# Optimization experiments

Measured on AMD Instinct MI355X. Metric: run time of the kernel, lower is better.

## Reference

```python
import jax, jax.numpy as jnp
import numpy as np

DEPTH, DIM, M_DIM, K = 3, 16, 16, 8  # depth, emb_dim, EGNN m_dim default, num_nearest_neighbors
LN_EPS = 1e-5


def _gather(x, idx):
    # x: [B,L,...], idx: [B,L,K] -> [B,L,K,...] (per-batch neighbor gather)
    return jax.vmap(lambda xb, ib: xb[ib])(x, idx)


def _lin(k, fi, fo):
    k1, k2 = jax.random.split(k)
    lim = 1.0 / np.sqrt(fi)
    w = jax.random.uniform(k1, (fi, fo), minval=-lim, maxval=lim, dtype=jnp.float32)
    b = jax.random.uniform(k2, (fo,), minval=-lim, maxval=lim, dtype=jnp.float32)
    return w, b


def _stacked(k, fi, fo):
    ws, bs = zip(*[_lin(kk, fi, fo) for kk in jax.random.split(k, DEPTH)])
    return jnp.stack(ws), jnp.stack(bs)


def setup_inputs() -> dict:
    key = jax.random.key(0)
    ks = jax.random.split(key, 16)
    B, L, num_tokens = 16, 1024, 2
    edge_in = 2 * DIM + 1  # feats_i, feats_j, rel_dist
    inp = {}
    inp['coords'] = jax.random.normal(ks[0], (B, L, 3), dtype=jnp.float32) * 3.0
    inp['residues'] = jax.random.randint(ks[1], (B, L), 0, num_tokens)
    inp['lengths'] = jax.random.randint(ks[2], (B,), L // 2, L + 1)
    inp['token_emb'] = jax.random.normal(ks[3], (num_tokens, DIM), dtype=jnp.float32)
    inp['pos_emb'] = jax.random.normal(ks[4], (L, DIM), dtype=jnp.float32)
    inp['edge_w1'], inp['edge_b1'] = _stacked(ks[5], edge_in, edge_in * 2)
    inp['edge_w2'], inp['edge_b2'] = _stacked(ks[6], edge_in * 2, M_DIM)
    inp['coors_w1'], inp['coors_b1'] = _stacked(ks[7], M_DIM, M_DIM * 4)
    inp['coors_w2'], inp['coors_b2'] = _stacked(ks[8], M_DIM * 4, 1)
    inp['ln_g'] = jnp.ones((DEPTH, DIM), jnp.float32)
    inp['ln_b'] = jnp.zeros((DEPTH, DIM), jnp.float32)
    inp['node_w1'], inp['node_b1'] = _stacked(ks[9], DIM + M_DIM, DIM * 2)
    inp['node_w2'], inp['node_b2'] = _stacked(ks[10], DIM * 2, DIM)
    inp['final_w'], inp['final_b'] = _lin(ks[11], DIM, 3)
    return inp


def reference(coords, residues, lengths, token_emb, pos_emb,
              edge_w1, edge_b1, edge_w2, edge_b2,
              coors_w1, coors_b1, coors_w2, coors_b2,
              ln_g, ln_b, node_w1, node_b1, node_w2, node_b2,
              final_w, final_b):
    B, L, _ = coords.shape
    silu = jax.nn.silu
    mask = jnp.arange(L)[None, :] < lengths[:, None]                 # [B,L]
    pair_mask = mask[:, :, None] & mask[:, None, :]                  # [B,L,L]
    eye = jnp.eye(L, dtype=bool)
    # chain adjacency: i <-> i+1 where both endpoints are within length
    r = jnp.arange(L - 1)
    chain = jnp.zeros((L, L), bool).at[r, r + 1].set(True)
    chain = chain | chain.T
    adj = (chain[None] & pair_mask) & ~eye                           # [B,L,L]

    feats = token_emb[residues] + pos_emb[None, :L]                  # [B,L,D]
    coors = coords
    for d in range(DEPTH):
        # pairwise squared distances for kNN ranking (memory-bound)
        rel_dist_full = jnp.sum((coors[:, :, None] - coors[:, None, :]) ** 2, -1)  # [B,L,L]
        ranking = jnp.where(pair_mask, rel_dist_full, 1e5)
        ranking = jnp.where(eye, -1.0, ranking)   # self always selected first
        ranking = jnp.where(adj, 0.0, ranking)    # adjacency edges forced in
        _, idx = jax.lax.top_k(-ranking, K)                           # [B,L,K] smallest
        mask_j = _gather(mask, idx)
        emask = mask[:, :, None] & mask_j                             # [B,L,K] (valid_radius=inf)
        coors_j = _gather(coors, idx)                                 # [B,L,K,3]
        rel_coors = coors[:, :, None] - coors_j                       # [B,L,K,3]
        rel_dist = jnp.sum(rel_coors ** 2, -1, keepdims=True)         # [B,L,K,1]
        feats_j = _gather(feats, idx)                                 # [B,L,K,D]
        feats_i = jnp.broadcast_to(feats[:, :, None], feats_j.shape)
        edge_in = jnp.concatenate([feats_i, feats_j, rel_dist], -1)   # [B,L,K,2D+1]
        h = silu(edge_in @ edge_w1[d] + edge_b1[d])
        m_ij = silu(h @ edge_w2[d] + edge_b2[d])                      # [B,L,K,M]
        # equivariant coordinate update
        w = silu(m_ij @ coors_w1[d] + coors_b1[d]) @ coors_w2[d] + coors_b2[d]
        w = jnp.where(emask[..., None], w, 0.0)[..., 0]               # [B,L,K]
        coors = coors + jnp.einsum('blk,blkc->blc', w, rel_coors)
        # node update (norm_feats=True in EGNN_Network -> LayerNorm)
        m_i = jnp.sum(jnp.where(emask[..., None], m_ij, 0.0), 2)      # [B,L,M]
        mu = feats.mean(-1, keepdims=True)
        var = jnp.mean((feats - mu) ** 2, -1, keepdims=True)
        normed = (feats - mu) / jnp.sqrt(var + LN_EPS) * ln_g[d] + ln_b[d]
        nin = jnp.concatenate([normed, m_i], -1)                      # [B,L,D+M]
        feats = feats + (silu(nin @ node_w1[d] + node_b1[d]) @ node_w2[d] + node_b2[d])
    delta = feats @ final_w + final_b                                 # [B,L,3]
    return delta
```

## Files before the change

### kernel.cpp

```cpp
#include <hip/hip_runtime.h>
#include <math.h>

typedef unsigned long long u64;
typedef unsigned int u32;

#define NB 16
#define SL 1024
#define DIM 16
#define MDIM 16
#define KNN 8
#define CH 64
#define NHID 32
#define LN_EPS 1e-5f
#define PST 144

__device__ __forceinline__ float silu_f(float x) {
    const float e = __expf(-x);
    return x * __builtin_amdgcn_rcpf(1.0f + e);
}

__global__ __launch_bounds__(256) void init_kernel(
    const float* __restrict__ coords, const int* __restrict__ residues,
    const float* __restrict__ token_emb, const float* __restrict__ pos_emb,
    const float* __restrict__ w1tp, const float* __restrict__ g_eb1,
    float* __restrict__ coordsA, float* __restrict__ featsA,
    float* __restrict__ Pout)
{
    const int t = blockIdx.x * 256 + threadIdx.x;
    const int node = t >> 2;
    const int part = t & 3;
    const int l = node & (SL - 1);
    const int r = residues[node];
    float f[16];
    {
        const float4* te = (const float4*)(token_emb + (size_t)r * DIM);
        const float4* pe = (const float4*)(pos_emb + (size_t)l * DIM);
#pragma unroll
        for (int q = 0; q < 4; ++q) {
            float4 a = te[q], b4 = pe[q];
            f[4*q+0] = a.x + b4.x; f[4*q+1] = a.y + b4.y;
            f[4*q+2] = a.z + b4.z; f[4*q+3] = a.w + b4.w;
        }
    }
    if (part == 0) {
        float4* fo = (float4*)(featsA + (size_t)node * DIM);
#pragma unroll
        for (int q = 0; q < 4; ++q)
            fo[q] = make_float4(f[4*q], f[4*q+1], f[4*q+2], f[4*q+3]);
        coordsA[node * 3 + 0] = coords[node * 3 + 0];
        coordsA[node * 3 + 1] = coords[node * 3 + 1];
        coordsA[node * 3 + 2] = coords[node * 3 + 2];
    }
    const int ubase = (part & 1) * 33;
    const int wbase = (part < 2) ? 0 : 66;
    float res[36];
    res[33] = 0.f; res[34] = 0.f; res[35] = 0.f;
#pragma unroll
    for (int oo = 0; oo < 33; ++oo) {
        const int u = ubase + oo;
        const float* wr = w1tp + (wbase + u) * 16;
        float a0 = (part < 2) ? g_eb1[u] : 0.0f;
        float a1 = 0.f, a2 = 0.f, a3 = 0.f;
#pragma unroll
        for (int c = 0; c < 16; c += 4) {
            a0 = fmaf(f[c + 0], wr[c + 0], a0);
            a1 = fmaf(f[c + 1], wr[c + 1], a1);
            a2 = fmaf(f[c + 2], wr[c + 2], a2);
            a3 = fmaf(f[c + 3], wr[c + 3], a3);
        }
        res[oo] = (a0 + a1) + (a2 + a3);
    }
    float4* op = (float4*)(Pout + (size_t)node * PST + part * 36);
#pragma unroll
    for (int q = 0; q < 9; ++q)
        op[q] = make_float4(res[4*q], res[4*q+1], res[4*q+2], res[4*q+3]);
}

__global__ __launch_bounds__(256) void pack_kernel(
    const float* __restrict__ ew1, const float* __restrict__ ew2,
    const float* __restrict__ cw1,
    const float* __restrict__ nw1, const float* __restrict__ nw2,
    float* __restrict__ w1tp, float* __restrict__ w1rp, float* __restrict__ w2p,
    float* __restrict__ cw1t, float* __restrict__ nw1t, float* __restrict__ nw2t)
{
    const int stride = gridDim.x * 256;
    const int t0 = blockIdx.x * 256 + threadIdx.x;
    for (int idx = t0; idx < 3 * 132 * 16; idx += stride) {
        int d = idx / (132 * 16); int r = idx - d * 132 * 16; int o = r >> 4; int c = r & 15;
        int u = (o < 66) ? o : (o - 66);
        int cc = (o < 66) ? c : (16 + c);
        w1tp[idx] = ew1[(d * 33 + cc) * 66 + u];
    }
    for (int idx = t0; idx < 3 * 72; idx += stride) {
        int d = idx / 72; int o = idx - d * 72; int hh = o / 36; int uu = o - hh * 36;
        w1rp[idx] = (uu < 33) ? ew1[(d * 33 + 32) * 66 + hh * 33 + uu] : 0.0f;
    }
    for (int idx = t0; idx < 3 * 72 * 16; idx += stride) {
        int d = idx / (72 * 16); int r = idx - d * 72 * 16; int u = r >> 4; int v = r & 15;
        int hh = u / 36; int uu = u - hh * 36;
        w2p[idx] = (uu < 33) ? ew2[(d * 66 + hh * 33 + uu) * 16 + v] : 0.0f;
    }
    for (int idx = t0; idx < 3 * CH * 16; idx += stride) {
        int d = idx / (CH * 16); int r = idx - d * CH * 16; int t = r >> 4; int v = r & 15;
        cw1t[(d * CH + t) * 16 + v] = cw1[(d * 16 + v) * CH + t];
    }
    for (int idx = t0; idx < 3 * NHID * 32; idx += stride) {
        int d = idx / (NHID * 32); int r = idx - d * NHID * 32; int u = r >> 5; int c = r & 31;
        nw1t[(d * NHID + u) * 32 + c] = nw1[(d * 32 + c) * NHID + u];
    }
    for (int idx = t0; idx < 3 * 16 * 32; idx += stride) {
        int d = idx / (16 * 32); int r = idx - d * 16 * 32; int c = r >> 5; int u = r & 31;
        nw2t[(d * 16 + c) * 32 + u] = nw2[(d * 32 + u) * 16 + c];
    }
}

__device__ __forceinline__ void merge8(u32* a, const u32* bb) {
    u32 c[8];
#pragma unroll
    for (int t = 0; t < 8; ++t) c[t] = min(a[t], bb[7 - t]);
#define MCAS(x, y) { u32 mn = min(c[x], c[y]); u32 mx = max(c[x], c[y]); c[x] = mn; c[y] = mx; }
    MCAS(0, 4) MCAS(1, 5) MCAS(2, 6) MCAS(3, 7)
    MCAS(0, 2) MCAS(1, 3) MCAS(4, 6) MCAS(5, 7)
    MCAS(0, 1) MCAS(2, 3) MCAS(4, 5) MCAS(6, 7)
#undef MCAS
#pragma unroll
    for (int t = 0; t < 8; ++t) a[t] = c[t];
}

__global__ __launch_bounds__(1024) void knn_kernel(
    const float* __restrict__ coords, const int* __restrict__ lengths,
    int* __restrict__ idxbuf)
{
    __shared__ __align__(16) float4 s_cand[SL];
    __shared__ u32 lists[16][64][9];
    const int tid = threadIdx.x;
    const int b = blockIdx.x >> 4;
    const int i0 = (blockIdx.x & 15) << 6;
    const int len = lengths[b];
    const float* cb = coords + (size_t)b * SL * 3;
    for (int idx = tid; idx < SL; idx += 1024) {
        const float* cp = cb + idx * 3;
        s_cand[idx] = make_float4(cp[0], cp[1], cp[2], 0.0f);
    }
    __syncthreads();

    const int wv = tid >> 6;
    const int lane = tid & 63;
    const int i = i0 + lane;
    const bool mi = i < len;
    const float4 qi = s_cand[i];
    const float xi = qi.x, yi = qi.y, zi = qi.z;

    u32 lst[8];
#pragma unroll
    for (int t = 0; t < 8; ++t) lst[t] = 0xFFFFFFFFu;

    const int jbase = wv << 6;
#pragma unroll 4
    for (int jj = 0; jj < 64; ++jj) {
        const int j = jbase + jj;
        const float4 cj = s_cand[j];
        const float dx = xi - cj.x, dy = yi - cj.y, dz = zi - cj.z;
        const float dist = dx * dx + dy * dy + dz * dz;
        const int dij = j - i;
        const bool pm = mi && (j < len);
        const bool adjx = (dij == 1) | (dij == -1);
        float v = pm ? (adjx ? 0.0f : dist) : 1e5f;
        v = (dij == 0) ? -1.0f : v;
        u32 bits = __float_as_uint(v);
        bits ^= (u32)((int)bits >> 31) | 0x80000000u;
        const u32 key = (bits & 0xFFFFFC00u) | (u32)j;
#pragma unroll
        for (int p = 7; p >= 1; --p)
            lst[p] = min(max(key, lst[p - 1]), lst[p]);
        lst[0] = min(key, lst[0]);
    }

#pragma unroll
    for (int t = 0; t < 8; ++t) lists[wv][lane][t] = lst[t];
    __syncthreads();

    if (tid < 512) {
        const int p = tid >> 6, q = tid & 63;
        u32 a[8], bb[8];
#pragma unroll
        for (int t = 0; t < 8; ++t) { a[t] = lists[2 * p][q][t]; bb[t] = lists[2 * p + 1][q][t]; }
        merge8(a, bb);
#pragma unroll
        for (int t = 0; t < 8; ++t) lists[2 * p][q][t] = a[t];
    }
    __syncthreads();
    if (tid < 256) {
        const int p = tid >> 6, q = tid & 63;
        u32 a[8], bb[8];
#pragma unroll
        for (int t = 0; t < 8; ++t) { a[t] = lists[4 * p][q][t]; bb[t] = lists[4 * p + 2][q][t]; }
        merge8(a, bb);
#pragma unroll
        for (int t = 0; t < 8; ++t) lists[4 * p][q][t] = a[t];
    }
    __syncthreads();
    if (tid < 128) {
        const int p = tid >> 6, q = tid & 63;
        u32 a[8], bb[8];
#pragma unroll
        for (int t = 0; t < 8; ++t) { a[t] = lists[8 * p][q][t]; bb[t] = lists[8 * p + 4][q][t]; }
        merge8(a, bb);
#pragma unroll
        for (int t = 0; t < 8; ++t) lists[8 * p][q][t] = a[t];
    }
    __syncthreads();
    if (tid < 64) {
        const int q = tid;
        u32 a[8], bb[8];
#pragma unroll
        for (int t = 0; t < 8; ++t) { a[t] = lists[0][q][t]; bb[t] = lists[8][q][t]; }
        merge8(a, bb);
        const size_t node = (size_t)b * SL + i0 + q;
        int4 r0 = make_int4((int)(a[0] & 1023u), (int)(a[1] & 1023u), (int)(a[2] & 1023u), (int)(a[3] & 1023u));
        int4 r1 = make_int4((int)(a[4] & 1023u), (int)(a[5] & 1023u), (int)(a[6] & 1023u), (int)(a[7] & 1023u));
        ((int4*)idxbuf)[node * 2 + 0] = r0;
        ((int4*)idxbuf)[node * 2 + 1] = r1;
    }
}

__global__ __launch_bounds__(256, 4) void layer_kernel(
    const int d,
    const float* __restrict__ coordsIn, float* __restrict__ coordsOut,
    const float* __restrict__ featsIn, float* __restrict__ featsOut,
    const float* __restrict__ Pbuf,
    const int* __restrict__ idxbuf, const int* __restrict__ lengths,
    const float* __restrict__ w1rp, const float* __restrict__ w2p,
    const float* __restrict__ g_eb2,
    const float* __restrict__ cw1t, const float* __restrict__ g_cb1,
    const float* __restrict__ g_cw2, const float* __restrict__ g_cb2,
    const float* __restrict__ g_lng, const float* __restrict__ g_lnb,
    const float* __restrict__ nw1t, const float* __restrict__ g_nb1,
    const float* __restrict__ nw2t, const float* __restrict__ g_nb2,
    const float* __restrict__ w1tp_all, const float* __restrict__ g_eb1,
    float* __restrict__ PbufOut)
{
    __shared__ float s_w2e[72 * 16];
    __shared__ float s_w1r[72];
    __shared__ float s_cw1[CH * 16];
    __shared__ float s_cw2v[CH];
    __shared__ float s_nw1[NHID * 36];
    __shared__ float s_nw2[16 * 36];
    __shared__ float s_eb2[16], s_cb1[CH];
    __shared__ float s_lng[16], s_lnb[16], s_nb1[32], s_nb2[16];
    __shared__ float s_cb2v;

    const int tid = threadIdx.x;
    for (int t = tid; t < 72 * 16; t += 256) s_w2e[t] = w2p[d * 72 * 16 + t];
    for (int t = tid; t < CH * 16; t += 256) s_cw1[t] = cw1t[d * CH * 16 + t];
    for (int t = tid; t < NHID * 32; t += 256) s_nw1[(t >> 5) * 36 + (t & 31)] = nw1t[d * NHID * 32 + t];
    for (int t = tid; t < 16 * 32; t += 256) s_nw2[(t >> 5) * 36 + (t & 31)] = nw2t[d * 16 * 32 + t];
    if (tid < 72) s_w1r[tid] = w1rp[d * 72 + tid];
    if (tid < CH) { s_cw2v[tid] = g_cw2[d * CH + tid]; s_cb1[tid] = g_cb1[d * CH + tid]; }
    if (tid < 16) {
        s_eb2[tid] = g_eb2[d * 16 + tid];
        s_lng[tid] = g_lng[d * 16 + tid];
        s_lnb[tid] = g_lnb[d * 16 + tid];
        s_nb2[tid] = g_nb2[d * 16 + tid];
    }
    if (tid < 32) s_nb1[tid] = g_nb1[d * 32 + tid];
    if (tid == 0) s_cb2v = g_cb2[d];

    const int lane = tid & 63;
    const int h = (lane >> 3) & 1;
    const int k = lane & 7;
    const int n = blockIdx.x * 16 + (tid >> 4);
    const int b = n >> 10;
    const int i = n & (SL - 1);
    const int len = lengths[b];
    const int j = idxbuf[n * 8 + k];
    const bool em = (i < len) && (j < len);

    float fi[16];
    {
        const float4* pp = (const float4*)(featsIn + (size_t)n * DIM);
        float4 a = pp[0], c2 = pp[1], c3 = pp[2], c4 = pp[3];
        fi[0]=a.x; fi[1]=a.y; fi[2]=a.z; fi[3]=a.w;
        fi[4]=c2.x; fi[5]=c2.y; fi[6]=c2.z; fi[7]=c2.w;
        fi[8]=c3.x; fi[9]=c3.y; fi[10]=c3.z; fi[11]=c3.w;
        fi[12]=c4.x; fi[13]=c4.y; fi[14]=c4.z; fi[15]=c4.w;
    }
    float ci[3], rel[3];
    {
        const float* cp = coordsIn + (size_t)n * 3;
        const float* cq = coordsIn + ((size_t)b * SL + j) * 3;
        ci[0] = cp[0]; ci[1] = cp[1]; ci[2] = cp[2];
        rel[0] = ci[0] - cq[0]; rel[1] = ci[1] - cq[1]; rel[2] = ci[2] - cq[2];
    }
    const float rd = fmaf(rel[0], rel[0], fmaf(rel[1], rel[1], rel[2] * rel[2]));

    const int ub = h * 36;
    const float* PiP = Pbuf + (size_t)n * PST + ub;
    const float* PjP = Pbuf + ((size_t)b * SL + j) * PST + 72 + ub;
    float4 pi_[9], pj_[9];
#pragma unroll
    for (int c4 = 0; c4 < 9; ++c4) {
        pi_[c4] = *(const float4*)(PiP + 4 * c4);
        pj_[c4] = *(const float4*)(PjP + 4 * c4);
    }

    __syncthreads();

    float macc[16];
#pragma unroll
    for (int v = 0; v < 16; ++v) macc[v] = h ? 0.0f : s_eb2[v];
#pragma unroll
    for (int c4 = 0; c4 < 9; ++c4) {
        const float4 pa = pi_[c4];
        const float4 pb = pj_[c4];
        const int u0 = ub + c4 * 4;
        const float hu0 = silu_f(fmaf(rd, s_w1r[u0 + 0], pa.x + pb.x));
        const float hu1 = silu_f(fmaf(rd, s_w1r[u0 + 1], pa.y + pb.y));
        const float hu2 = silu_f(fmaf(rd, s_w1r[u0 + 2], pa.z + pb.z));
        const float hu3 = silu_f(fmaf(rd, s_w1r[u0 + 3], pa.w + pb.w));
        const float* w2r = &s_w2e[u0 * 16];
#pragma unroll
        for (int v = 0; v < 16; ++v) {
            float m0 = fmaf(hu0, w2r[v], macc[v]);
            float m1 = fmaf(hu1, w2r[16 + v], m0);
            float m2 = fmaf(hu2, w2r[32 + v], m1);
            macc[v] = fmaf(hu3, w2r[48 + v], m2);
        }
    }

    float mm[16];
#pragma unroll
    for (int v = 0; v < 16; ++v)
        mm[v] = silu_f(macc[v] + __shfl_xor(macc[v], 8, 64));

    const int tb = h * 32;
    float wa = 0.f;
#pragma unroll 4
    for (int tt = 0; tt < 32; ++tt) {
        const float* cr = &s_cw1[(tb + tt) * 16];
        float a0 = s_cb1[tb + tt], a1 = 0.f;
#pragma unroll
        for (int v = 0; v < 16; v += 2) {
            a0 = fmaf(mm[v], cr[v], a0);
            a1 = fmaf(mm[v + 1], cr[v + 1], a1);
        }
        wa = fmaf(silu_f(a0 + a1), s_cw2v[tb + tt], wa);
    }
    const float wao = __shfl_xor(wa, 8, 64);
    const float we = em ? (wa + wao + s_cb2v) : 0.f;

    float wr0 = we * rel[0], wr1 = we * rel[1], wr2 = we * rel[2];
#pragma unroll
    for (int s = 1; s < 8; s <<= 1) {
        wr0 += __shfl_xor(wr0, s, 64);
        wr1 += __shfl_xor(wr1, s, 64);
        wr2 += __shfl_xor(wr2, s, 64);
    }
    if ((lane & 15) == 0) {
        coordsOut[(size_t)n * 3 + 0] = ci[0] + wr0;
        coordsOut[(size_t)n * 3 + 1] = ci[1] + wr1;
        coordsOut[(size_t)n * 3 + 2] = ci[2] + wr2;
    }

    float mi_[16];
#pragma unroll
    for (int v = 0; v < 16; ++v) mi_[v] = em ? mm[v] : 0.f;
#pragma unroll
    for (int s = 1; s < 8; s <<= 1) {
#pragma unroll
        for (int v = 0; v < 16; ++v) mi_[v] += __shfl_xor(mi_[v], s, 64);
    }

    float mu = 0.f;
#pragma unroll
    for (int c = 0; c < 16; ++c) mu += fi[c];
    mu *= 0.0625f;
    float var = 0.f;
#pragma unroll
    for (int c = 0; c < 16; ++c) { const float dd = fi[c] - mu; var = fmaf(dd, dd, var); }
    var *= 0.0625f;
    const float rs = rsqrtf(var + LN_EPS);
    float nn[16];
#pragma unroll
    for (int c = 0; c < 16; ++c) nn[c] = fmaf((fi[c] - mu) * rs, s_lng[c], s_lnb[c]);

    const int sub = lane & 15;
    float nh[2];
#pragma unroll
    for (int q = 0; q < 2; ++q) {
        const int u = sub * 2 + q;
        const float* nr = &s_nw1[u * 36];
        float a0 = s_nb1[u], a1 = 0.f;
#pragma unroll
        for (int c = 0; c < 16; c += 2) {
            a0 = fmaf(nn[c], nr[c], a0);
            a1 = fmaf(nn[c + 1], nr[c + 1], a1);
        }
#pragma unroll
        for (int v = 0; v < 16; v += 2) {
            a0 = fmaf(mi_[v], nr[16 + v], a0);
            a1 = fmaf(mi_[v + 1], nr[16 + v + 1], a1);
        }
        nh[q] = silu_f(a0 + a1);
    }

    const int nbase = lane & ~15;
    const float* w2c = &s_nw2[sub * 36];
    float o0 = s_nb2[sub];
#pragma unroll
    for (int u = 0; u < 32; ++u) {
        const float v = __shfl(nh[u & 1], nbase + (u >> 1), 64);
        o0 = fmaf(v, w2c[u], o0);
    }
    const float fo = fi[sub] + o0;
    featsOut[(size_t)n * DIM + sub] = fo;

    if (d < 2) {
        float fr[16];
#pragma unroll
        for (int c = 0; c < 16; ++c) fr[c] = __shfl(fo, nbase + c, 64);
        const float* wbase = w1tp_all + (d + 1) * 132 * 16;
        const float* bbase = g_eb1 + (d + 1) * 66;
        float* Pout = PbufOut + (size_t)n * PST;
#pragma unroll
        for (int q = 0; q < 9; ++q) {
            const int col = sub + (q << 4);
            const int ch = (col >= 108) ? 3 : (col >= 72) ? 2 : (col >= 36) ? 1 : 0;
            const int uu = col - ch * 36;
            const bool valid = uu < 33;
            const int u = ((ch & 1) ? 33 : 0) + uu;
            const int uc = valid ? u : 0;
            const int widx = valid ? ((ch < 2) ? u : 66 + u) : 0;
            float a0 = (valid && ch < 2) ? bbase[uc] : 0.0f;
            float a1 = 0.f, a2 = 0.f, a3 = 0.f;
            const float* wr = wbase + widx * 16;
#pragma unroll
            for (int cc = 0; cc < 16; cc += 4) {
                a0 = fmaf(fr[cc + 0], wr[cc + 0], a0);
                a1 = fmaf(fr[cc + 1], wr[cc + 1], a1);
                a2 = fmaf(fr[cc + 2], wr[cc + 2], a2);
                a3 = fmaf(fr[cc + 3], wr[cc + 3], a3);
            }
            Pout[col] = valid ? ((a0 + a1) + (a2 + a3)) : 0.0f;
        }
    }
}

__global__ __launch_bounds__(256) void final_kernel(
    const float* __restrict__ feats, const float* __restrict__ fw,
    const float* __restrict__ fb, float* __restrict__ out)
{
    const int nid = blockIdx.x * 256 + threadIdx.x;
    if (nid >= NB * SL) return;
    float f[DIM];
#pragma unroll
    for (int c = 0; c < DIM; ++c) f[c] = feats[nid * DIM + c];
#pragma unroll
    for (int o = 0; o < 3; ++o) {
        float acc = fb[o];
#pragma unroll
        for (int c = 0; c < DIM; ++c) acc = fmaf(f[c], fw[c * 3 + o], acc);
        out[nid * 3 + o] = acc;
    }
}

extern "C" void kernel_launch(void* const* d_in, const int* in_sizes, int n_in,
                              void* d_out, int out_size, void* d_ws, size_t ws_size,
                              hipStream_t stream) {
    const float* coords    = (const float*)d_in[0];
    const int*   residues  = (const int*)d_in[1];
    const int*   lengths   = (const int*)d_in[2];
    const float* token_emb = (const float*)d_in[3];
    const float* pos_emb   = (const float*)d_in[4];
    const float* ew1 = (const float*)d_in[5];
    const float* eb1 = (const float*)d_in[6];
    const float* ew2 = (const float*)d_in[7];
    const float* eb2 = (const float*)d_in[8];
    const float* cw1 = (const float*)d_in[9];
    const float* cb1 = (const float*)d_in[10];
    const float* cw2 = (const float*)d_in[11];
    const float* cb2 = (const float*)d_in[12];
    const float* lng = (const float*)d_in[13];
    const float* lnb = (const float*)d_in[14];
    const float* nw1 = (const float*)d_in[15];
    const float* nb1 = (const float*)d_in[16];
    const float* nw2 = (const float*)d_in[17];
    const float* nb2 = (const float*)d_in[18];
    const float* fw  = (const float*)d_in[19];
    const float* fb  = (const float*)d_in[20];

    float* ws = (float*)d_ws;
    float* coordsA = ws;
    float* coordsB = coordsA + NB * SL * 3;
    float* featsA  = coordsB + NB * SL * 3;
    float* featsB  = featsA + NB * SL * DIM;
    int*   idxbuf  = (int*)(featsB + NB * SL * DIM);
    float* w1tp = (float*)(idxbuf + NB * SL * KNN);
    float* w1rp = w1tp + 3 * 132 * 16;
    float* w2p  = w1rp + 3 * 72;
    float* cw1t = w2p + 3 * 72 * 16;
    float* nw1t = cw1t + 3 * CH * 16;
    float* nw2t = nw1t + 3 * NHID * 32;
    float* PbufA = nw2t + 3 * 16 * 32;
    float* PbufB = PbufA + (size_t)NB * SL * PST;

    pack_kernel<<<32, 256, 0, stream>>>(ew1, ew2, cw1, nw1, nw2, w1tp, w1rp, w2p, cw1t, nw1t, nw2t);
    init_kernel<<<NB * SL * 4 / 256, 256, 0, stream>>>(coords, residues, token_emb, pos_emb,
                                                        w1tp, eb1, coordsA, featsA, PbufA);

    float* cIn = coordsA; float* cOut = coordsB;
    float* fIn = featsA;  float* fOut = featsB;
    float* pIn = PbufA;   float* pOut = PbufB;
    for (int d = 0; d < 3; ++d) {
        knn_kernel<<<NB * SL / 64, 1024, 0, stream>>>(cIn, lengths, idxbuf);
        layer_kernel<<<NB * SL * KNN / 128, 256, 0, stream>>>(d, cIn, cOut, fIn, fOut, pIn, idxbuf, lengths,
            w1rp, w2p, eb2, cw1t, cb1, cw2, cb2, lng, lnb, nw1t, nb1, nw2t, nb2,
            w1tp, eb1, pOut);
        float* t;
        t = cIn; cIn = cOut; cOut = t;
        t = fIn; fIn = fOut; fOut = t;
        t = pIn; pIn = pOut; pOut = t;
    }

    final_kernel<<<NB * SL / 256, 256, 0, stream>>>(fIn, fw, fb, (float*)d_out);
}
```

Before: 281.2 us.

## Process two nodes per thread group in layer kernel to reuse shared weights

Each 16-lane group now handles two nodes (A and B, 16 apart), so every weight read from shared memory is reused for two independent FMA chains, and the grid is halved. The P-buffer float4 loads move into the compute loop and the w1r row is read as one aligned float4. This cuts LDS traffic per edge and adds independent work to hide latency. The cost is roughly double register use under launch_bounds(256,4), which may cause spills or lower occupancy, and fewer blocks.

```diff
diff --git a/kernel.cpp b/kernel.cpp
--- a/kernel.cpp
+++ b/kernel.cpp
@@ -241,7 +241,7 @@
     float* __restrict__ PbufOut)
 {
     __shared__ float s_w2e[72 * 16];
-    __shared__ float s_w1r[72];
+    __shared__ __align__(16) float s_w1r[72];
     __shared__ float s_cw1[CH * 16];
     __shared__ float s_cw2v[CH];
     __shared__ float s_nw1[NHID * 36];
@@ -269,159 +269,230 @@
     const int lane = tid & 63;
     const int h = (lane >> 3) & 1;
     const int k = lane & 7;
-    const int n = blockIdx.x * 16 + (tid >> 4);
-    const int b = n >> 10;
-    const int i = n & (SL - 1);
+    const int sub = lane & 15;
+    const int nA = blockIdx.x * 32 + (tid >> 4);
+    const int nB = nA + 16;
+    const int b = nA >> 10;
     const int len = lengths[b];
-    const int j = idxbuf[n * 8 + k];
-    const bool em = (i < len) && (j < len);
-
-    float fi[16];
+    const int jA = idxbuf[nA * 8 + k];
+    const int jB = idxbuf[nB * 8 + k];
+    const bool emA = ((nA & 1023) < len) && (jA < len);
+    const bool emB = ((nB & 1023) < len) && (jB < len);
+
+    float ciA[3], relA[3], ciB[3], relB[3];
     {
-        const float4* pp = (const float4*)(featsIn + (size_t)n * DIM);
-        float4 a = pp[0], c2 = pp[1], c3 = pp[2], c4 = pp[3];
-        fi[0]=a.x; fi[1]=a.y; fi[2]=a.z; fi[3]=a.w;
-        fi[4]=c2.x; fi[5]=c2.y; fi[6]=c2.z; fi[7]=c2.w;
-        fi[8]=c3.x; fi[9]=c3.y; fi[10]=c3.z; fi[11]=c3.w;
-        fi[12]=c4.x; fi[13]=c4.y; fi[14]=c4.z; fi[15]=c4.w;
-    }
-    float ci[3], rel[3];
-    {
-        const float* cp = coordsIn + (size_t)n * 3;
-        const float* cq = coordsIn + ((size_t)b * SL + j) * 3;
-        ci[0] = cp[0]; ci[1] = cp[1]; ci[2] = cp[2];
-        rel[0] = ci[0] - cq[0]; rel[1] = ci[1] - cq[1]; rel[2] = ci[2] - cq[2];
-    }
-    const float rd = fmaf(rel[0], rel[0], fmaf(rel[1], rel[1], rel[2] * rel[2]));
+        const float* cpA = coordsIn + (size_t)nA * 3;
+        const float* cqA = coordsIn + ((size_t)b * SL + jA) * 3;
+        ciA[0] = cpA[0]; ciA[1] = cpA[1]; ciA[2] = cpA[2];
+        relA[0] = ciA[0] - cqA[0]; relA[1] = ciA[1] - cqA[1]; relA[2] = ciA[2] - cqA[2];
+        const float* cpB = coordsIn + (size_t)nB * 3;
+        const float* cqB = coordsIn + ((size_t)b * SL + jB) * 3;
+        ciB[0] = cpB[0]; ciB[1] = cpB[1]; ciB[2] = cpB[2];
+        relB[0] = ciB[0] - cqB[0]; relB[1] = ciB[1] - cqB[1]; relB[2] = ciB[2] - cqB[2];
+    }
+    const float rdA = fmaf(relA[0], relA[0], fmaf(relA[1], relA[1], relA[2] * relA[2]));
+    const float rdB = fmaf(relB[0], relB[0], fmaf(relB[1], relB[1], relB[2] * relB[2]));
 
     const int ub = h * 36;
-    const float* PiP = Pbuf + (size_t)n * PST + ub;
-    const float* PjP = Pbuf + ((size_t)b * SL + j) * PST + 72 + ub;
-    float4 pi_[9], pj_[9];
+    const float* PiA = Pbuf + (size_t)nA * PST + ub;
+    const float* PjA = Pbuf + ((size_t)b * SL + jA) * PST + 72 + ub;
+    const float* PiB = Pbuf + (size_t)nB * PST + ub;
+    const float* PjB = Pbuf + ((size_t)b * SL + jB) * PST + 72 + ub;
+
+    __syncthreads();
+
+    float maccA[16], maccB[16];
+#pragma unroll
+    for (int v = 0; v < 16; ++v) {
+        const float e0 = h ? 0.0f : s_eb2[v];
+        maccA[v] = e0; maccB[v] = e0;
+    }
 #pragma unroll
     for (int c4 = 0; c4 < 9; ++c4) {
-        pi_[c4] = *(const float4*)(PiP + 4 * c4);
-        pj_[c4] = *(const float4*)(PjP + 4 * c4);
-    }
-
-    __syncthreads();
-
-    float macc[16];
-#pragma unroll
-    for (int v = 0; v < 16; ++v) macc[v] = h ? 0.0f : s_eb2[v];
-#pragma unroll
-    for (int c4 = 0; c4 < 9; ++c4) {
-        const float4 pa = pi_[c4];
-        const float4 pb = pj_[c4];
+        const float4 paA = *(const float4*)(PiA + 4 * c4);
+        const float4 pbA = *(const float4*)(PjA + 4 * c4);
+        const float4 paB = *(const float4*)(PiB + 4 * c4);
+        const float4 pbB = *(const float4*)(PjB + 4 * c4);
         const int u0 = ub + c4 * 4;
-        const float hu0 = silu_f(fmaf(rd, s_w1r[u0 + 0], pa.x + pb.x));
-        const float hu1 = silu_f(fmaf(rd, s_w1r[u0 + 1], pa.y + pb.y));
-        const float hu2 = silu_f(fmaf(rd, s_w1r[u0 + 2], pa.z + pb.z));
-        const float hu3 = silu_f(fmaf(rd, s_w1r[u0 + 3], pa.w + pb.w));
+        const float4 w1r4 = *(const float4*)&s_w1r[u0];
+        const float huA0 = silu_f(fmaf(rdA, w1r4.x, paA.x + pbA.x));
+        const float huA1 = silu_f(fmaf(rdA, w1r4.y, paA.y + pbA.y));
+        const float huA2 = silu_f(fmaf(rdA, w1r4.z, paA.z + pbA.z));
+        const float huA3 = silu_f(fmaf(rdA, w1r4.w, paA.w + pbA.w));
+        const float huB0 = silu_f(fmaf(rdB, w1r4.x, paB.x + pbB.x));
+        const float huB1 = silu_f(fmaf(rdB, w1r4.y, paB.y + pbB.y));
+        const float huB2 = silu_f(fmaf(rdB, w1r4.z, paB.z + pbB.z));
+        const float huB3 = silu_f(fmaf(rdB, w1r4.w, paB.w + pbB.w));
         const float* w2r = &s_w2e[u0 * 16];
 #pragma unroll
         for (int v = 0; v < 16; ++v) {
-            float m0 = fmaf(hu0, w2r[v], macc[v]);
-            float m1 = fmaf(hu1, w2r[16 + v], m0);
-            float m2 = fmaf(hu2, w2r[32 + v], m1);
-            macc[v] = fmaf(hu3, w2r[48 + v], m2);
-        }
-    }
-
-    float mm[16];
-#pragma unroll
-    for (int v = 0; v < 16; ++v)
-        mm[v] = silu_f(macc[v] + __shfl_xor(macc[v], 8, 64));
+            const float w0 = w2r[v], w1 = w2r[16 + v], w2_ = w2r[32 + v], w3 = w2r[48 + v];
+            maccA[v] = fmaf(huA3, w3, fmaf(huA2, w2_, fmaf(huA1, w1, fmaf(huA0, w0, maccA[v]))));
+            maccB[v] = fmaf(huB3, w3, fmaf(huB2, w2_, fmaf(huB1, w1, fmaf(huB0, w0, maccB[v]))));
+        }
+    }
+
+    float mmA[16], mmB[16];
+#pragma unroll
+    for (int v = 0; v < 16; ++v) {
+        mmA[v] = silu_f(maccA[v] + __shfl_xor(maccA[v], 8, 64));
+        mmB[v] = silu_f(maccB[v] + __shfl_xor(maccB[v], 8, 64));
+    }
 
     const int tb = h * 32;
-    float wa = 0.f;
+    float waA = 0.f, waB = 0.f;
 #pragma unroll 4
     for (int tt = 0; tt < 32; ++tt) {
         const float* cr = &s_cw1[(tb + tt) * 16];
-        float a0 = s_cb1[tb + tt], a1 = 0.f;
+        const float bias = s_cb1[tb + tt];
+        float a0A = bias, a1A = 0.f, a0B = bias, a1B = 0.f;
 #pragma unroll
         for (int v = 0; v < 16; v += 2) {
-            a0 = fmaf(mm[v], cr[v], a0);
-            a1 = fmaf(mm[v + 1], cr[v + 1], a1);
-        }
-        wa = fmaf(silu_f(a0 + a1), s_cw2v[tb + tt], wa);
-    }
-    const float wao = __shfl_xor(wa, 8, 64);
-    const float we = em ? (wa + wao + s_cb2v) : 0.f;
-
-    float wr0 = we * rel[0], wr1 = we * rel[1], wr2 = we * rel[2];
+            a0A = fmaf(mmA[v], cr[v], a0A);
+            a1A = fmaf(mmA[v + 1], cr[v + 1], a1A);
+            a0B = fmaf(mmB[v], cr[v], a0B);
+            a1B = fmaf(mmB[v + 1], cr[v + 1], a1B);
+        }
+        const float cw2v = s_cw2v[tb + tt];
+        waA = fmaf(silu_f(a0A + a1A), cw2v, waA);
+        waB = fmaf(silu_f(a0B + a1B), cw2v, waB);
+    }
+    const float waoA = __shfl_xor(waA, 8, 64);
+    const float waoB = __shfl_xor(waB, 8, 64);
+    const float weA = emA ? (waA + waoA + s_cb2v) : 0.f;
+    const float weB = emB ? (waB + waoB + s_cb2v) : 0.f;
+
+    float wr0A = weA * relA[0], wr1A = weA * relA[1], wr2A = weA * relA[2];
+    float wr0B = weB * relB[0], wr1B = weB * relB[1], wr2B = weB * relB[2];
 #pragma unroll
     for (int s = 1; s < 8; s <<= 1) {
-        wr0 += __shfl_xor(wr0, s, 64);
-        wr1 += __shfl_xor(wr1, s, 64);
-        wr2 += __shfl_xor(wr2, s, 64);
+        wr0A += __shfl_xor(wr0A, s, 64);
+        wr1A += __shfl_xor(wr1A, s, 64);
+        wr2A += __shfl_xor(wr2A, s, 64);
+        wr0B += __shfl_xor(wr0B, s, 64);
+        wr1B += __shfl_xor(wr1B, s, 64);
+        wr2B += __shfl_xor(wr2B, s, 64);
     }
     if ((lane & 15) == 0) {
-        coordsOut[(size_t)n * 3 + 0] = ci[0] + wr0;
-        coordsOut[(size_t)n * 3 + 1] = ci[1] + wr1;
-        coordsOut[(size_t)n * 3 + 2] = ci[2] + wr2;
-    }
-
-    float mi_[16];
-#pragma unroll
-    for (int v = 0; v < 16; ++v) mi_[v] = em ? mm[v] : 0.f;
+        coordsOut[(size_t)nA * 3 + 0] = ciA[0] + wr0A;
+        coordsOut[(size_t)nA * 3 + 1] = ciA[1] + wr1A;
+        coordsOut[(size_t)nA * 3 + 2] = ciA[2] + wr2A;
+        coordsOut[(size_t)nB * 3 + 0] = ciB[0] + wr0B;
+        coordsOut[(size_t)nB * 3 + 1] = ciB[1] + wr1B;
+        coordsOut[(size_t)nB * 3 + 2] = ciB[2] + wr2B;
+    }
+
+    float fiA[16], fiB[16];
+    {
+        const float4* ppA = (const float4*)(featsIn + (size_t)nA * DIM);
+        float4 a0 = ppA[0], a1 = ppA[1], a2 = ppA[2], a3 = ppA[3];
+        fiA[0]=a0.x; fiA[1]=a0.y; fiA[2]=a0.z; fiA[3]=a0.w;
+        fiA[4]=a1.x; fiA[5]=a1.y; fiA[6]=a1.z; fiA[7]=a1.w;
+        fiA[8]=a2.x; fiA[9]=a2.y; fiA[10]=a2.z; fiA[11]=a2.w;
+        fiA[12]=a3.x; fiA[13]=a3.y; fiA[14]=a3.z; fiA[15]=a3.w;
+        const float4* ppB = (const float4*)(featsIn + (size_t)nB * DIM);
+        float4 b0 = ppB[0], b1 = ppB[1], b2 = ppB[2], b3 = ppB[3];
+        fiB[0]=b0.x; fiB[1]=b0.y; fiB[2]=b0.z; fiB[3]=b0.w;
+        fiB[4]=b1.x; fiB[5]=b1.y; fiB[6]=b1.z; fiB[7]=b1.w;
+        fiB[8]=b2.x; fiB[9]=b2.y; fiB[10]=b2.z; fiB[11]=b2.w;
+        fiB[12]=b3.x; fiB[13]=b3.y; fiB[14]=b3.z; fiB[15]=b3.w;
+    }
+    const float fiSubA = featsIn[(size_t)nA * DIM + sub];
+    const float fiSubB = featsIn[(size_t)nB * DIM + sub];
+
+    float miA[16], miB[16];
+#pragma unroll
+    for (int v = 0; v < 16; ++v) {
+        miA[v] = emA ? mmA[v] : 0.f;
+        miB[v] = emB ? mmB[v] : 0.f;
+    }
 #pragma unroll
     for (int s = 1; s < 8; s <<= 1) {
 #pragma unroll
-        for (int v = 0; v < 16; ++v) mi_[v] += __shfl_xor(mi_[v], s, 64);
-    }
-
-    float mu = 0.f;
-#pragma unroll
-    for (int c = 0; c < 16; ++c) mu += fi[c];
-    mu *= 0.0625f;
-    float var = 0.f;
-#pragma unroll
-    for (int c = 0; c < 16; ++c) { const float dd = fi[c] - mu; var = fmaf(dd, dd, var); }
-    var *= 0.0625f;
-    const float rs = rsqrtf(var + LN_EPS);
-    float nn[16];
-#pragma unroll
-    for (int c = 0; c < 16; ++c) nn[c] = fmaf((fi[c] - mu) * rs, s_lng[c], s_lnb[c]);
-
-    const int sub = lane & 15;
-    float nh[2];
+        for (int v = 0; v < 16; ++v) {
+            miA[v] += __shfl_xor(miA[v], s, 64);
+            miB[v] += __shfl_xor(miB[v], s, 64);
+        }
+    }
+
+    float nnA[16], nnB[16];
+    {
+        float mu = 0.f;
+#pragma unroll
+        for (int c = 0; c < 16; ++c) mu += fiA[c];
+        mu *= 0.0625f;
+        float var = 0.f;
+#pragma unroll
+        for (int c = 0; c < 16; ++c) { const float dd = fiA[c] - mu; var = fmaf(dd, dd, var); }
+        var *= 0.0625f;
+        const float rs = rsqrtf(var + LN_EPS);
+#pragma unroll
+        for (int c = 0; c < 16; ++c) nnA[c] = fmaf((fiA[c] - mu) * rs, s_lng[c], s_lnb[c]);
+    }
+    {
+        float mu = 0.f;
+#pragma unroll
+        for (int c = 0; c < 16; ++c) mu += fiB[c];
+        mu *= 0.0625f;
+        float var = 0.f;
+#pragma unroll
+        for (int c = 0; c < 16; ++c) { const float dd = fiB[c] - mu; var = fmaf(dd, dd, var); }
+        var *= 0.0625f;
+        const float rs = rsqrtf(var + LN_EPS);
+#pragma unroll
+        for (int c = 0; c < 16; ++c) nnB[c] = fmaf((fiB[c] - mu) * rs, s_lng[c], s_lnb[c]);
+    }
+
+    float nhA[2], nhB[2];
 #pragma unroll
     for (int q = 0; q < 2; ++q) {
         const int u = sub * 2 + q;
         const float* nr = &s_nw1[u * 36];
-        float a0 = s_nb1[u], a1 = 0.f;
+        const float bias = s_nb1[u];
+        float a0A = bias, a1A = 0.f, a0B = bias, a1B = 0.f;
 #pragma unroll
         for (int c = 0; c < 16; c += 2) {
-            a0 = fmaf(nn[c], nr[c], a0);
-            a1 = fmaf(nn[c + 1], nr[c + 1], a1);
+            a0A = fmaf(nnA[c], nr[c], a0A);
+            a1A = fmaf(nnA[c + 1], nr[c + 1], a1A);
+            a0B = fmaf(nnB[c], nr[c], a0B);
+            a1B = fmaf(nnB[c + 1], nr[c + 1], a1B);
         }
 #pragma unroll
         for (int v = 0; v < 16; v += 2) {
-            a0 = fmaf(mi_[v], nr[16 + v], a0);
-            a1 = fmaf(mi_[v + 1], nr[16 + v + 1], a1);
-        }
-        nh[q] = silu_f(a0 + a1);
+            a0A = fmaf(miA[v], nr[16 + v], a0A);
+            a1A = fmaf(miA[v + 1], nr[16 + v + 1], a1A);
+            a0B = fmaf(miB[v], nr[16 + v], a0B);
+            a1B = fmaf(miB[v + 1], nr[16 + v + 1], a1B);
+        }
+        nhA[q] = silu_f(a0A + a1A);
+        nhB[q] = silu_f(a0B + a1B);
     }
 
     const int nbase = lane & ~15;
     const float* w2c = &s_nw2[sub * 36];
-    float o0 = s_nb2[sub];
+    float oA = s_nb2[sub], oB = s_nb2[sub];
 #pragma unroll
     for (int u = 0; u < 32; ++u) {
-        const float v = __shfl(nh[u & 1], nbase + (u >> 1), 64);
-        o0 = fmaf(v, w2c[u], o0);
-    }
-    const float fo = fi[sub] + o0;
-    featsOut[(size_t)n * DIM + sub] = fo;
+        const float w = w2c[u];
+        oA = fmaf(__shfl(nhA[u & 1], nbase + (u >> 1), 64), w, oA);
+        oB = fmaf(__shfl(nhB[u & 1], nbase + (u >> 1), 64), w, oB);
+    }
+    const float foA = fiSubA + oA;
+    const float foB = fiSubB + oB;
+    featsOut[(size_t)nA * DIM + sub] = foA;
+    featsOut[(size_t)nB * DIM + sub] = foB;
 
     if (d < 2) {
-        float fr[16];
-#pragma unroll
-        for (int c = 0; c < 16; ++c) fr[c] = __shfl(fo, nbase + c, 64);
+        float frA[16], frB[16];
+#pragma unroll
+        for (int c = 0; c < 16; ++c) {
+            frA[c] = __shfl(foA, nbase + c, 64);
+            frB[c] = __shfl(foB, nbase + c, 64);
+        }
         const float* wbase = w1tp_all + (d + 1) * 132 * 16;
         const float* bbase = g_eb1 + (d + 1) * 66;
-        float* Pout = PbufOut + (size_t)n * PST;
+        float* PoutA = PbufOut + (size_t)nA * PST;
+        float* PoutB = PbufOut + (size_t)nB * PST;
 #pragma unroll
         for (int q = 0; q < 9; ++q) {
             const int col = sub + (q << 4);
@@ -431,17 +502,24 @@
             const int u = ((ch & 1) ? 33 : 0) + uu;
             const int uc = valid ? u : 0;
             const int widx = valid ? ((ch < 2) ? u : 66 + u) : 0;
-            float a0 = (valid && ch < 2) ? bbase[uc] : 0.0f;
-            float a1 = 0.f, a2 = 0.f, a3 = 0.f;
+            const float bias = (valid && ch < 2) ? bbase[uc] : 0.0f;
+            float a0A = bias, a1A = 0.f, a2A = 0.f, a3A = 0.f;
+            float a0B = bias, a1B = 0.f, a2B = 0.f, a3B = 0.f;
             const float* wr = wbase + widx * 16;
 #pragma unroll
             for (int cc = 0; cc < 16; cc += 4) {
-                a0 = fmaf(fr[cc + 0], wr[cc + 0], a0);
-                a1 = fmaf(fr[cc + 1], wr[cc + 1], a1);
-                a2 = fmaf(fr[cc + 2], wr[cc + 2], a2);
-                a3 = fmaf(fr[cc + 3], wr[cc + 3], a3);
+                const float w0 = wr[cc + 0], w1 = wr[cc + 1], w2_ = wr[cc + 2], w3 = wr[cc + 3];
+                a0A = fmaf(frA[cc + 0], w0, a0A);
+                a1A = fmaf(frA[cc + 1], w1, a1A);
+                a2A = fmaf(frA[cc + 2], w2_, a2A);
+                a3A = fmaf(frA[cc + 3], w3, a3A);
+                a0B = fmaf(frB[cc + 0], w0, a0B);
+                a1B = fmaf(frB[cc + 1], w1, a1B);
+                a2B = fmaf(frB[cc + 2], w2_, a2B);
+                a3B = fmaf(frB[cc + 3], w3, a3B);
             }
-            Pout[col] = valid ? ((a0 + a1) + (a2 + a3)) : 0.0f;
+            PoutA[col] = valid ? ((a0A + a1A) + (a2A + a3A)) : 0.0f;
+            PoutB[col] = valid ? ((a0B + a1B) + (a2B + a3B)) : 0.0f;
         }
     }
 }
@@ -513,7 +591,7 @@
     float* pIn = PbufA;   float* pOut = PbufB;
     for (int d = 0; d < 3; ++d) {
         knn_kernel<<<NB * SL / 64, 1024, 0, stream>>>(cIn, lengths, idxbuf);
-        layer_kernel<<<NB * SL * KNN / 128, 256, 0, stream>>>(d, cIn, cOut, fIn, fOut, pIn, idxbuf, lengths,
+        layer_kernel<<<NB * SL * KNN / 256, 256, 0, stream>>>(d, cIn, cOut, fIn, fOut, pIn, idxbuf, lengths,
             w1rp, w2p, eb2, cw1t, cb1, cw2, cb2, lng, lnb, nw1t, nb1, nw2t, nb2,
             w1tp, eb1, pOut);
         float* t;
```

After: 286.6 us. About the same (+1.9%).
